# Performance work log

Measured on AMD Instinct MI355X. Metric: run time of the kernel, lower is better.

Reference implementation:

```python
import jax, jax.numpy as jnp
import numpy as np

B, N, D, H = 1, 4096, 1024, 16
HD = D // H  # head_dim = 64


def setup_inputs() -> dict:
    key = jax.random.key(0)
    ks = jax.random.split(key, 5)
    s = 0.02
    return {
        "x": jax.random.normal(ks[0], (B, N, D), dtype=jnp.float32),
        "Wq": jax.random.normal(ks[1], (D, D), dtype=jnp.float32) * s,
        "Wk": jax.random.normal(ks[2], (D, D), dtype=jnp.float32) * s,
        "Wv": jax.random.normal(ks[3], (D, D), dtype=jnp.float32) * s,
        "Wo": jax.random.normal(ks[4], (D, D), dtype=jnp.float32) * s,
        "bo": jnp.zeros((D,), dtype=jnp.float32),
    }


def reference(x, Wq, Wk, Wv, Wo, bo):
    b, n, d = x.shape
    # QKV projections -> [b, h, n, hd]
    def proj(W):
        return jnp.einsum("bnd,de->bne", x, W).reshape(b, n, H, HD).transpose(0, 2, 1, 3)
    q, k, v = proj(Wq), proj(Wk), proj(Wv)
    # Scores [b, h, n, n] with causal mask (matches masked_fill with triu(diag=1))
    scores = jnp.einsum("bhqd,bhkd->bhqk", q, k)
    causal = jnp.tril(jnp.ones((n, n), dtype=bool))
    scores = jnp.where(causal, scores, -jnp.inf)
    attn = jax.nn.softmax(scores / jnp.sqrt(jnp.float32(HD)), axis=-1)
    # dropout p=0.0 -> identity
    ctx = jnp.einsum("bhqk,bhkd->bhqd", attn, v)
    ctx = ctx.transpose(0, 2, 1, 3).reshape(b, n, d)
    return jnp.einsum("bnd,de->bne", ctx, Wo) + bo
```

## Files before the change

kernel.cpp:

```cpp
#include <hip/hip_runtime.h>


#define N_TOK 4096
#define DMODEL 1024
#define NH 16
#define HDIM 64

typedef __bf16 bf16x8 __attribute__((ext_vector_type(8)));
typedef __bf16 bf16x2v __attribute__((ext_vector_type(2)));
typedef short short4v __attribute__((ext_vector_type(4)));
typedef unsigned int uint2v __attribute__((ext_vector_type(2)));
typedef float f32x4 __attribute__((ext_vector_type(4)));

__device__ __forceinline__ unsigned short f2bf(float f) {
  unsigned u = __builtin_bit_cast(unsigned, f);
  u += 0x7FFFu + ((u >> 16) & 1u);
  return (unsigned short)(u >> 16);
}

__device__ __forceinline__ float bf2f(unsigned short u) {
  unsigned x = (unsigned)u << 16;
  return __builtin_bit_cast(float, x);
}

__device__ __forceinline__ unsigned pack2bf(float f0, float f1) {
  unsigned a = __builtin_bit_cast(unsigned, f0);
  unsigned b = __builtin_bit_cast(unsigned, f1);
  a += 0x7FFFu + ((a >> 16) & 1u);
  b += 0x7FFFu + ((b >> 16) & 1u);
  return (a >> 16) | (b & 0xFFFF0000u);
}

__device__ __forceinline__ unsigned packpk(float f0, float f1) {
#if defined(__HIP_DEVICE_COMPILE__) && __has_builtin(__builtin_amdgcn_cvt_pk_bf16_f32)
  bf16x2v r = __builtin_amdgcn_cvt_pk_bf16_f32(f0, f1);
  return __builtin_bit_cast(unsigned, r);
#else
  return pack2bf(f0, f1);
#endif
}

__device__ __forceinline__ float fast_exp2(float x) {
#if defined(__HIP_DEVICE_COMPILE__)
#if __has_builtin(__builtin_amdgcn_exp2f)
  return __builtin_amdgcn_exp2f(x);
#else
  float r;
  asm("v_exp_f32 %0, %1" : "=v"(r) : "v"(x));
  return r;
#endif
#else
  return exp2f(x);
#endif
}

__device__ __forceinline__ f32x4 mfma16x16x16(short4v a, short4v b, f32x4 c) {
#if defined(__HIP_DEVICE_COMPILE__)
#if __has_builtin(__builtin_amdgcn_mfma_f32_16x16x16bf16_1k)
  return __builtin_amdgcn_mfma_f32_16x16x16bf16_1k(a, b, c, 0, 0, 0);
#else
  asm volatile("v_mfma_f32_16x16x16_bf16 %0, %1, %2, %0\n\ts_nop 7\n\ts_nop 1"
               : "+v"(c) : "v"(a), "v"(b));
  return c;
#endif
#else
  return c;
#endif
}

__device__ __forceinline__ void gll16(const unsigned short* g, unsigned short* l) {
#if defined(__HIP_DEVICE_COMPILE__)
  __builtin_amdgcn_global_load_lds((const __attribute__((address_space(1))) void*)g,
                                   (__attribute__((address_space(3))) void*)l, 16, 0, 0);
#endif
}

__global__ __launch_bounds__(256) void prep_kernel(
    const float* __restrict__ x, unsigned short* __restrict__ xb,
    const float* __restrict__ Wq, const float* __restrict__ Wk,
    const float* __restrict__ Wv, const float* __restrict__ Wo,
    unsigned short* __restrict__ Wqt, unsigned short* __restrict__ Wkt,
    unsigned short* __restrict__ Wvt, unsigned short* __restrict__ Wot) {
  const int bx = blockIdx.x;
  if (bx < 4096) {
    const int i = (bx * 256 + threadIdx.x) * 4;
    float4 v = *(const float4*)(x + i);
    ushort4 o;
    o.x = f2bf(v.x); o.y = f2bf(v.y); o.z = f2bf(v.z); o.w = f2bf(v.w);
    *(ushort4*)(xb + i) = o;
    return;
  }
  __shared__ float t[32][33];
  const int r = bx - 4096;
  const int z = r >> 10, rem = r & 1023;
  const int by = rem >> 5, bxx = rem & 31;
  const float* src;
  unsigned short* dst;
  switch (z) {
    case 0: src = Wq; dst = Wqt; break;
    case 1: src = Wk; dst = Wkt; break;
    case 2: src = Wv; dst = Wvt; break;
    default: src = Wo; dst = Wot; break;
  }
  const int tx = threadIdx.x & 31, ty = threadIdx.x >> 5;
  const int xx = bxx * 32 + tx;
  const int y0 = by * 32;
#pragma unroll
  for (int i = 0; i < 32; i += 8) t[ty + i][tx] = src[(y0 + ty + i) * DMODEL + xx];
  __syncthreads();
  const int ox = by * 32 + tx;
  const int oy0 = bxx * 32;
#pragma unroll
  for (int i = 0; i < 32; i += 8) dst[(oy0 + ty + i) * DMODEL + ox] = f2bf(t[tx][ty + i]);
}

__global__ __launch_bounds__(256) void gemm_qkv_kernel(
    const unsigned short* __restrict__ xb,
    const unsigned short* __restrict__ Wqt, const unsigned short* __restrict__ Wkt,
    const unsigned short* __restrict__ Wvt,
    unsigned short* __restrict__ Qg, unsigned short* __restrict__ Kg,
    unsigned short* __restrict__ Vtg) {
  __shared__ __align__(16) char smem[32768];
  const int z = blockIdx.z;
  const unsigned short* Bmat = (z == 0) ? Wqt : ((z == 1) ? Wkt : Wvt);
  const int tid = threadIdx.x, lane = tid & 63, wv = tid >> 6;
  const int quad = lane >> 4, l15 = lane & 15;
  const int wm = wv >> 1, wn = wv & 1;
  const int tm0 = blockIdx.y * 128, tn0 = blockIdx.x * 128;
  const int lrow = lane >> 2, lcol = (lane & 3) * 8;
  const f32x4 zero4 = {0.f, 0.f, 0.f, 0.f};
  f32x4 acc[4][4];
#pragma unroll
  for (int i = 0; i < 4; ++i)
#pragma unroll
    for (int j = 0; j < 4; ++j) acc[i][j] = zero4;

  auto stage = [&](int kb, int b) {
    unsigned short* As = (unsigned short*)(smem + b * 16384);
    unsigned short* Bs = (unsigned short*)(smem + b * 16384 + 8192);
#pragma unroll
    for (int r = 0; r < 2; ++r) {
      const int row0 = r * 64 + wv * 16;
      gll16(&xb[(tm0 + row0 + lrow) * DMODEL + kb + lcol], &As[row0 * 32]);
      gll16(&Bmat[(tn0 + row0 + lrow) * DMODEL + kb + lcol], &Bs[row0 * 32]);
    }
  };

  stage(0, 0);
  stage(32, 1);
  int cur = 0;
#pragma unroll 1
  for (int kb = 0; kb < DMODEL; kb += 32) {
    if (kb + 32 < DMODEL) asm volatile("s_waitcnt vmcnt(4)" ::: "memory");
    else                  asm volatile("s_waitcnt vmcnt(0)" ::: "memory");
    __builtin_amdgcn_s_barrier();
    const unsigned short* As = (const unsigned short*)(smem + cur * 16384);
    const unsigned short* Bs = (const unsigned short*)(smem + cur * 16384 + 8192);
    bf16x8 af[4], bfr[4];
#pragma unroll
    for (int i = 0; i < 4; ++i) {
      af[i]  = *(const bf16x8*)&As[(wm * 64 + i * 16 + l15) * 32 + quad * 8];
      bfr[i] = *(const bf16x8*)&Bs[(wn * 64 + i * 16 + l15) * 32 + quad * 8];
    }
#pragma unroll
    for (int mt = 0; mt < 4; ++mt)
#pragma unroll
      for (int nt = 0; nt < 4; ++nt)
        acc[mt][nt] = __builtin_amdgcn_mfma_f32_16x16x32_bf16(af[mt], bfr[nt], acc[mt][nt], 0, 0, 0);
    if (kb + 64 < DMODEL) {
      __builtin_amdgcn_s_barrier();
      stage(kb + 64, cur);
    }
    cur ^= 1;
  }
  __syncthreads();

  const float qs = 0.125f * 1.44269504088896f;
  if (z < 2) {
#pragma unroll
    for (int mt = 0; mt < 4; ++mt)
#pragma unroll
      for (int nt = 0; nt < 4; ++nt)
#pragma unroll
        for (int r = 0; r < 4; ++r) {
          const int row = tm0 + wm * 64 + mt * 16 + quad * 4 + r;
          const int col = tn0 + wn * 64 + nt * 16 + l15;
          const float v = acc[mt][nt][r];
          const int hh = col >> 6, hd = col & 63;
          if (z == 0) Qg[(hh * N_TOK + row) * HDIM + hd] = f2bf(v * qs);
          else        Kg[(hh * N_TOK + row) * HDIM + hd] = f2bf(v);
        }
  } else {
    unsigned short* Tt = (unsigned short*)smem;
#pragma unroll 1
    for (int p = 0; p < 2; ++p) {
      if (wn == p) {
#pragma unroll
        for (int mt = 0; mt < 4; ++mt)
#pragma unroll
          for (int nt = 0; nt < 4; ++nt) {
            const int c = nt * 16 + l15;
#pragma unroll
            for (int r = 0; r < 4; ++r)
              Tt[c * 132 + wm * 64 + mt * 16 + quad * 4 + r] = f2bf(acc[mt][nt][r]);
          }
      }
      __syncthreads();
      const int c = tid >> 2, seg = tid & 3;
      const int hh = (tn0 + p * 64) >> 6;
      unsigned short* dst = Vtg + hh * (HDIM * N_TOK) + c * N_TOK + tm0 + seg * 32;
      const unsigned short* srcp = &Tt[c * 132 + seg * 32];
#pragma unroll
      for (int j = 0; j < 4; ++j)
        *(uint4*)(dst + j * 8) = *(const uint4*)(srcp + j * 8);
      __syncthreads();
    }
  }
}

#define TRW 68

__device__ static const unsigned char T_TAB[80] = {
    7, 14, 15, 15, 21, 22, 22, 23, 23, 23, 28, 29, 29, 30, 30, 30, 31, 31, 31, 31,
    6, 12, 13, 13, 14, 18, 19, 19, 20, 20, 20, 21, 21, 22, 24, 25, 25, 26, 26, 26,
    27, 27, 27, 27, 28, 28, 28, 29, 29, 30,
    5, 10, 11, 11, 12, 16, 16, 17, 17, 17, 18, 18, 19, 24, 24, 24, 25, 25, 26,
    4, 8, 9, 9, 10, 16,
    3, 8,
    2,
    1,
    0};
__device__ static const unsigned char G_TAB[80] = {
    0, 0, 0, 1, 0, 0, 1, 0, 1, 2, 0, 0, 1, 0, 1, 2, 0, 1, 2, 3,
    0, 0, 0, 1, 1, 0, 0, 1, 0, 1, 2, 1, 2, 2, 0, 0, 1, 0, 1, 2,
    0, 1, 2, 3, 1, 2, 3, 2, 3, 3,
    0, 0, 0, 1, 1, 0, 1, 0, 1, 2, 1, 2, 2, 1, 2, 3, 2, 3, 3,
    0, 0, 0, 1, 1, 2,
    0, 1,
    0,
    0,
    0};
__device__ static const unsigned char PS_TAB[32] = {
    0, 0, 0, 0, 0, 0, 0, 0,
    0, 2, 4, 6, 8, 10, 12, 14,
    16, 19, 22, 25, 28, 31, 34, 37,
    40, 44, 48, 52, 56, 60, 64, 68};

__device__ __forceinline__ unsigned short* part_slot_ptr(
    unsigned short* poA, unsigned short* poB, int slot) {
  return (slot < 384) ? poA + (size_t)slot * 8192
                      : poB + (size_t)(slot - 384) * 8192;
}

__device__ __forceinline__ void stage_kv(
    const unsigned short* __restrict__ Kh, const unsigned short* __restrict__ Vh,
    int kv0, char* buf, int wv, int lane) {
  unsigned short* Ksb = (unsigned short*)buf;
  unsigned short* Vsb = (unsigned short*)(buf + 8192);
  const int r8 = lane >> 3, g = lane & 7;
  const int sw = ((g ^ r8) * 8);
#pragma unroll
  for (int i = 0; i < 2; ++i) {
    const int row = wv * 16 + i * 8;
    gll16(&Kh[(kv0 + row + r8) * HDIM + sw], &Ksb[row * 64]);
    gll16(&Vh[(row + r8) * N_TOK + kv0 + sw], &Vsb[row * 64]);
  }
}

template <bool MASKED>
__device__ __forceinline__ void attn_step(
    int kvs, int qw, int quad, int l15,
    const unsigned short* __restrict__ Ks, const unsigned short* __restrict__ Vs,
    const bf16x8 (&qf)[2][2], f32x4 (&o)[2][4], float (&l_)[2]) {
  const f32x4 zero4 = {0.f, 0.f, 0.f, 0.f};
  const int s = l15 & 7;
  f32x4 c[2][4];
#pragma unroll
  for (int mt = 0; mt < 4; ++mt) {
    const unsigned short* kp = &Ks[(mt * 16 + l15) * 64];
    const int g0 = (quad ^ s) * 8;
    const bf16x8 kf0 = *(const bf16x8*)(kp + g0);
    const bf16x8 kf1 = *(const bf16x8*)(kp + (g0 ^ 32));
#pragma unroll
    for (int qt = 0; qt < 2; ++qt) {
      c[qt][mt] = __builtin_amdgcn_mfma_f32_16x16x32_bf16(kf0, qf[qt][0], zero4, 0, 0, 0);
      c[qt][mt] = __builtin_amdgcn_mfma_f32_16x16x32_bf16(kf1, qf[qt][1], c[qt][mt], 0, 0, 0);
    }
  }
  short4v pb[2][4];
#pragma unroll
  for (int qt = 0; qt < 2; ++qt) {
    const int q = qw + qt * 16 + l15;
    float ls = 0.f;
#pragma unroll
    for (int mt = 0; mt < 4; ++mt) {
      float p[4];
#pragma unroll
      for (int r = 0; r < 4; ++r) {
        float v = c[qt][mt][r];
        if (MASKED) v = ((kvs + mt * 16 + quad * 4 + r) <= q) ? v : -3e38f;
        p[r] = fast_exp2(v);
      }
      ls += (p[0] + p[1]) + (p[2] + p[3]);
      uint2v w;
      w.x = packpk(p[0], p[1]);
      w.y = packpk(p[2], p[3]);
      pb[qt][mt] = __builtin_bit_cast(short4v, w);
    }
    l_[qt] += ls;
  }
#pragma unroll
  for (int mt = 0; mt < 4; ++mt)
#pragma unroll
    for (int dt = 0; dt < 4; ++dt) {
      const int gv = (((2 * mt + (quad >> 1)) ^ s) * 8) + (quad & 1) * 4;
      const short4v vfx = *(const short4v*)&Vs[(dt * 16 + l15) * 64 + gv];
      o[0][dt] = mfma16x16x16(vfx, pb[0][mt], o[0][dt]);
      o[1][dt] = mfma16x16x16(vfx, pb[1][mt], o[1][dt]);
    }
}

__global__ __launch_bounds__(256, 4) void attn_kernel(
    const unsigned short* __restrict__ Qg, const unsigned short* __restrict__ Kg,
    const unsigned short* __restrict__ Vtg, unsigned short* __restrict__ ctx,
    unsigned short* __restrict__ part_oA, unsigned short* __restrict__ part_oB,
    float* __restrict__ part_l) {
  __shared__ __align__(16) char smem[34816];
  const int tid = threadIdx.x, lane = tid & 63, wv = tid >> 6;
  const int quad = lane >> 4, l15 = lane & 15;

  const int xcd = blockIdx.x & 7;
  const int iblk = blockIdx.x >> 3;
  const int h = (xcd << 1) | (iblk & 1);
  const int u = iblk >> 1;
  const int t = T_TAB[u], g = G_TAB[u];
  const int ng = (t >> 3) + 1;
  const int tp1 = t + 1;
  const int gbase = tp1 / ng;
  const int grem = tp1 - gbase * ng;
  const int s0 = g * gbase + (g < grem ? g : grem);
  const int cnt = gbase + (g < grem ? 1 : 0);
  const int mlen = 2 * cnt;
  const bool multi = (t >= 8);
  const int qb = t * 128, qw = qb + wv * 32;

  const unsigned short* Qh = Qg + h * N_TOK * HDIM;
  const unsigned short* Kh = Kg + h * N_TOK * HDIM;
  const unsigned short* Vh = Vtg + h * HDIM * N_TOK;

  bf16x8 qf[2][2];
#pragma unroll
  for (int qt = 0; qt < 2; ++qt)
#pragma unroll
    for (int hh = 0; hh < 2; ++hh)
      qf[qt][hh] = *(const bf16x8*)&Qh[(qw + qt * 16 + l15) * HDIM + hh * 32 + quad * 8];

  const f32x4 zero4 = {0.f, 0.f, 0.f, 0.f};
  f32x4 o[2][4];
#pragma unroll
  for (int qt = 0; qt < 2; ++qt)
#pragma unroll
    for (int dt = 0; dt < 4; ++dt) o[qt][dt] = zero4;
  float l_[2] = {0.f, 0.f};

  const int kvbase = s0 << 7;
  stage_kv(Kh, Vh, kvbase, smem, wv, lane);
  stage_kv(Kh, Vh, kvbase + 64, smem + 16384, wv, lane);
  int cur = 0;
#pragma unroll 1
  for (int mc = 0; mc < mlen; ++mc) {
    const int kv0 = kvbase + mc * 64;
    if (mc + 1 < mlen) asm volatile("s_waitcnt vmcnt(4)" ::: "memory");
    else               asm volatile("s_waitcnt vmcnt(0)" ::: "memory");
    __builtin_amdgcn_s_barrier();
    const unsigned short* Ksb = (const unsigned short*)(smem + cur * 16384);
    const unsigned short* Vsb = (const unsigned short*)(smem + cur * 16384 + 8192);
    if (kv0 <= qw + 31) {
      __builtin_amdgcn_s_setprio(1);
      if (kv0 + 63 <= qw)
        attn_step<false>(kv0, qw, quad, l15, Ksb, Vsb, qf, o, l_);
      else
        attn_step<true>(kv0, qw, quad, l15, Ksb, Vsb, qf, o, l_);
      __builtin_amdgcn_s_setprio(0);
    }
    if (mc + 2 < mlen) {
      __builtin_amdgcn_s_barrier();
      stage_kv(Kh, Vh, kv0 + 128, smem + cur * 16384, wv, lane);
    }
    cur ^= 1;
  }
  __syncthreads();

  float* Tr = (float*)(smem + wv * (16 * TRW * 4));
  const int tq = lane >> 2, seg = lane & 3;
  if (!multi) {
#pragma unroll
    for (int qt = 0; qt < 2; ++qt) {
      float l = l_[qt];
      l += __shfl_xor(l, 16, 64);
      l += __shfl_xor(l, 32, 64);
      const float inv = 1.0f / l;
#pragma unroll
      for (int dt = 0; dt < 4; ++dt) {
        f32x4 v = o[qt][dt] * inv;
        *(f32x4*)&Tr[l15 * TRW + dt * 16 + quad * 4] = v;
      }
      unsigned short* dst = &ctx[(qb + wv * 32 + qt * 16 + tq) * DMODEL + h * HDIM + seg * 16];
      const float* src = &Tr[tq * TRW + seg * 16];
#pragma unroll
      for (int j = 0; j < 2; ++j) {
        const float* s8 = src + j * 8;
        uint4 w;
        w.x = pack2bf(s8[0], s8[1]);
        w.y = pack2bf(s8[2], s8[3]);
        w.z = pack2bf(s8[4], s8[5]);
        w.w = pack2bf(s8[6], s8[7]);
        *(uint4*)(dst + j * 8) = w;
      }
    }
  } else {
    const int slot = h * 72 + PS_TAB[t] + g;
    unsigned short* pobase = part_slot_ptr(part_oA, part_oB, slot);
#pragma unroll
    for (int qt = 0; qt < 2; ++qt) {
      float l = l_[qt];
      l += __shfl_xor(l, 16, 64);
      l += __shfl_xor(l, 32, 64);
      if (quad == 0) part_l[slot * 128 + wv * 32 + qt * 16 + l15] = l;
#pragma unroll
      for (int dt = 0; dt < 4; ++dt)
        *(f32x4*)&Tr[l15 * TRW + dt * 16 + quad * 4] = o[qt][dt];
      unsigned short* dst = pobase + (wv * 32 + qt * 16 + tq) * 64 + seg * 16;
      const float* src = &Tr[tq * TRW + seg * 16];
#pragma unroll
      for (int j = 0; j < 2; ++j) {
        const float* s8 = src + j * 8;
        uint4 w;
        w.x = pack2bf(s8[0], s8[1]);
        w.y = pack2bf(s8[2], s8[3]);
        w.z = pack2bf(s8[4], s8[5]);
        w.w = pack2bf(s8[6], s8[7]);
        *(uint4*)(dst + j * 8) = w;
      }
    }
  }
}

__global__ __launch_bounds__(256) void merge_kernel(
    unsigned short* __restrict__ part_oA, unsigned short* __restrict__ part_oB,
    const float* __restrict__ part_l, unsigned short* __restrict__ ctx) {
  const int b = blockIdx.x;
  const int h = b / 24, tt = b - h * 24;
  const int t = tt + 8;
  const int ng = (t >> 3) + 1;
  const int tid = threadIdx.x;
  const int q = tid >> 1, half = tid & 1;
  const int slot0 = h * 72 + PS_TAB[t];
  float l = 0.f;
  for (int g = 0; g < ng; ++g) l += part_l[(slot0 + g) * 128 + q];
  const float inv = 1.0f / l;
  unsigned short* dst = &ctx[(t * 128 + q) * DMODEL + h * HDIM + half * 32];
#pragma unroll
  for (int j = 0; j < 4; ++j) {
    float acc[8] = {0.f, 0.f, 0.f, 0.f, 0.f, 0.f, 0.f, 0.f};
    for (int g = 0; g < ng; ++g) {
      const unsigned short* po = part_slot_ptr(part_oA, part_oB, slot0 + g);
      const uint4 w = *(const uint4*)(po + q * 64 + half * 32 + j * 8);
      const unsigned short* us = (const unsigned short*)&w;
#pragma unroll
      for (int e = 0; e < 8; ++e) acc[e] += bf2f(us[e]);
    }
    uint4 w;
    w.x = pack2bf(acc[0] * inv, acc[1] * inv);
    w.y = pack2bf(acc[2] * inv, acc[3] * inv);
    w.z = pack2bf(acc[4] * inv, acc[5] * inv);
    w.w = pack2bf(acc[6] * inv, acc[7] * inv);
    *(uint4*)(dst + j * 8) = w;
  }
}

__global__ __launch_bounds__(256) void gemm_out_kernel(
    const unsigned short* __restrict__ ctxb, const unsigned short* __restrict__ Wot,
    const float* __restrict__ bo, float* __restrict__ out) {
  __shared__ __align__(16) char smem[24576];
  const int tid = threadIdx.x, lane = tid & 63, wv = tid >> 6;
  const int quad = lane >> 4, l15 = lane & 15;
  const int wm = wv >> 1, wn = wv & 1;
  const int tm0 = blockIdx.y * 128, tn0 = blockIdx.x * 64;
  const int lrow = lane >> 2, lcol = (lane & 3) * 8;
  const f32x4 zero4 = {0.f, 0.f, 0.f, 0.f};
  f32x4 acc[4][2];
#pragma unroll
  for (int i = 0; i < 4; ++i)
#pragma unroll
    for (int j = 0; j < 2; ++j) acc[i][j] = zero4;

  auto stage = [&](int kb, int b) {
    unsigned short* As = (unsigned short*)(smem + b * 8192);
    unsigned short* Bs = (unsigned short*)(smem + 16384 + b * 4096);
    const int ra = wv * 32;
    gll16(&ctxb[(tm0 + ra + lrow) * DMODEL + kb + lcol], &As[ra * 32]);
    gll16(&ctxb[(tm0 + ra + 16 + lrow) * DMODEL + kb + lcol], &As[(ra + 16) * 32]);
    const int rb = wv * 16;
    gll16(&Wot[(tn0 + rb + lrow) * DMODEL + kb + lcol], &Bs[rb * 32]);
  };
  stage(0, 0);
  stage(32, 1);
  int cur = 0;
#pragma unroll 1
  for (int kb = 0; kb < DMODEL; kb += 32) {
    if (kb + 32 < DMODEL) asm volatile("s_waitcnt vmcnt(3)" ::: "memory");
    else                  asm volatile("s_waitcnt vmcnt(0)" ::: "memory");
    __builtin_amdgcn_s_barrier();
    const unsigned short* As = (const unsigned short*)(smem + cur * 8192);
    const unsigned short* Bs = (const unsigned short*)(smem + 16384 + cur * 4096);
    bf16x8 af[4], bfr[2];
#pragma unroll
    for (int i = 0; i < 4; ++i)
      af[i] = *(const bf16x8*)&As[(wm * 64 + i * 16 + l15) * 32 + quad * 8];
#pragma unroll
    for (int j = 0; j < 2; ++j)
      bfr[j] = *(const bf16x8*)&Bs[(wn * 32 + j * 16 + l15) * 32 + quad * 8];
#pragma unroll
    for (int mt = 0; mt < 4; ++mt)
#pragma unroll
      for (int nt = 0; nt < 2; ++nt)
        acc[mt][nt] = __builtin_amdgcn_mfma_f32_16x16x32_bf16(af[mt], bfr[nt], acc[mt][nt], 0, 0, 0);
    if (kb + 64 < DMODEL) {
      __builtin_amdgcn_s_barrier();
      stage(kb + 64, cur);
    }
    cur ^= 1;
  }
#pragma unroll
  for (int mt = 0; mt < 4; ++mt)
#pragma unroll
    for (int nt = 0; nt < 2; ++nt)
#pragma unroll
      for (int r = 0; r < 4; ++r) {
        const int row = tm0 + wm * 64 + mt * 16 + quad * 4 + r;
        const int col = tn0 + wn * 32 + nt * 16 + l15;
        out[row * DMODEL + col] = acc[mt][nt][r] + bo[col];
      }
}

extern "C" void kernel_launch(void* const* d_in, const int* in_sizes, int n_in,
                              void* d_out, int out_size, void* d_ws, size_t ws_size,
                              hipStream_t stream) {
  const float* x  = (const float*)d_in[0];
  const float* Wq = (const float*)d_in[1];
  const float* Wk = (const float*)d_in[2];
  const float* Wv = (const float*)d_in[3];
  const float* Wo = (const float*)d_in[4];
  const float* bo = (const float*)d_in[5];
  float* out = (float*)d_out;

  char* ws = (char*)d_ws;
  unsigned short* xb  = (unsigned short*)(ws);
  unsigned short* Wqt = (unsigned short*)(ws + 8388608);
  unsigned short* Wkt = (unsigned short*)(ws + 8388608 + 2097152);
  unsigned short* Wvt = (unsigned short*)(ws + 8388608 + 2 * 2097152);
  unsigned short* Wot = (unsigned short*)(ws + 8388608 + 3 * 2097152);
  unsigned short* Qg  = (unsigned short*)(ws + 16777216);
  unsigned short* Kg  = (unsigned short*)(ws + 25165824);
  unsigned short* Vtg = (unsigned short*)(ws + 33554432);
  unsigned short* ctx = xb;
  unsigned short* part_oA = (unsigned short*)(ws + 8388608);
  unsigned short* part_oB = (unsigned short*)(ws + 41943040);
  float* part_l = (float*)(ws + 54525952);

  prep_kernel<<<8192, 256, 0, stream>>>(x, xb, Wq, Wk, Wv, Wo, Wqt, Wkt, Wvt, Wot);
  gemm_qkv_kernel<<<dim3(DMODEL / 128, N_TOK / 128, 3), 256, 0, stream>>>(xb, Wqt, Wkt, Wvt, Qg, Kg, Vtg);
  attn_kernel<<<1280, 256, 0, stream>>>(Qg, Kg, Vtg, ctx, part_oA, part_oB, part_l);
  merge_kernel<<<384, 256, 0, stream>>>(part_oA, part_oB, part_l, ctx);
  gemm_out_kernel<<<dim3(DMODEL / 64, N_TOK / 128), 256, 0, stream>>>(ctx, Wot, bo, out);
}
```

Measured before the change: 206.2 us.

## Fuse x fp32-to-bf16 conversion into QKV GEMM A-tile loading

The separate pass that converts x to bf16 in the prep kernel is removed. The QKV GEMM now loads fp32 x tiles into registers, packs them to bf16 and writes them to LDS, software-pipelined one stage ahead. The weight B tiles keep using global_load_lds. This drops one full read/write round trip of x through HBM and halves the prep launch, but every GEMM block now reads fp32 A data (twice the bytes, repeated across column blocks and z) and spends VALU and LDS writes on the conversion. It also adds a launch_bounds occupancy hint of 3.

Measured after the change: 204.1 us. About the same (-1.0%).

```diff
diff --git a/kernel.cpp b/kernel.cpp
--- a/kernel.cpp
+++ b/kernel.cpp
@@ -76,22 +76,12 @@
 }
 
 __global__ __launch_bounds__(256) void prep_kernel(
-    const float* __restrict__ x, unsigned short* __restrict__ xb,
     const float* __restrict__ Wq, const float* __restrict__ Wk,
     const float* __restrict__ Wv, const float* __restrict__ Wo,
     unsigned short* __restrict__ Wqt, unsigned short* __restrict__ Wkt,
     unsigned short* __restrict__ Wvt, unsigned short* __restrict__ Wot) {
-  const int bx = blockIdx.x;
-  if (bx < 4096) {
-    const int i = (bx * 256 + threadIdx.x) * 4;
-    float4 v = *(const float4*)(x + i);
-    ushort4 o;
-    o.x = f2bf(v.x); o.y = f2bf(v.y); o.z = f2bf(v.z); o.w = f2bf(v.w);
-    *(ushort4*)(xb + i) = o;
-    return;
-  }
   __shared__ float t[32][33];
-  const int r = bx - 4096;
+  const int r = blockIdx.x;
   const int z = r >> 10, rem = r & 1023;
   const int by = rem >> 5, bxx = rem & 31;
   const float* src;
@@ -114,8 +104,8 @@
   for (int i = 0; i < 32; i += 8) dst[(oy0 + ty + i) * DMODEL + ox] = f2bf(t[tx][ty + i]);
 }
 
-__global__ __launch_bounds__(256) void gemm_qkv_kernel(
-    const unsigned short* __restrict__ xb,
+__global__ __launch_bounds__(256, 3) void gemm_qkv_kernel(
+    const float* __restrict__ x,
     const unsigned short* __restrict__ Wqt, const unsigned short* __restrict__ Wkt,
     const unsigned short* __restrict__ Wvt,
     unsigned short* __restrict__ Qg, unsigned short* __restrict__ Kg,
@@ -135,24 +125,45 @@
 #pragma unroll
     for (int j = 0; j < 4; ++j) acc[i][j] = zero4;
 
-  auto stage = [&](int kb, int b) {
+  const int arow = tid >> 1;
+  const int ahalf = (tid & 1) << 4;
+  const float* xrow = x + (size_t)(tm0 + arow) * DMODEL + ahalf;
+  float4 a0, a1, a2, a3;
+  auto issueA = [&](int kb) {
+    const float* p = xrow + kb;
+    a0 = *(const float4*)(p);
+    a1 = *(const float4*)(p + 4);
+    a2 = *(const float4*)(p + 8);
+    a3 = *(const float4*)(p + 12);
+  };
+  auto writeA = [&](int b) {
     unsigned short* As = (unsigned short*)(smem + b * 16384);
+    uint4 w0, w1;
+    w0.x = packpk(a0.x, a0.y); w0.y = packpk(a0.z, a0.w);
+    w0.z = packpk(a1.x, a1.y); w0.w = packpk(a1.z, a1.w);
+    w1.x = packpk(a2.x, a2.y); w1.y = packpk(a2.z, a2.w);
+    w1.z = packpk(a3.x, a3.y); w1.w = packpk(a3.z, a3.w);
+    *(uint4*)&As[arow * 32 + ahalf] = w0;
+    *(uint4*)&As[arow * 32 + ahalf + 8] = w1;
+  };
+  auto stageB = [&](int kb, int b) {
     unsigned short* Bs = (unsigned short*)(smem + b * 16384 + 8192);
 #pragma unroll
     for (int r = 0; r < 2; ++r) {
       const int row0 = r * 64 + wv * 16;
-      gll16(&xb[(tm0 + row0 + lrow) * DMODEL + kb + lcol], &As[row0 * 32]);
       gll16(&Bmat[(tn0 + row0 + lrow) * DMODEL + kb + lcol], &Bs[row0 * 32]);
     }
   };
 
-  stage(0, 0);
-  stage(32, 1);
+  stageB(0, 0);
+  stageB(32, 1);
+  issueA(0);
+  writeA(0);
+  issueA(32);
   int cur = 0;
 #pragma unroll 1
   for (int kb = 0; kb < DMODEL; kb += 32) {
-    if (kb + 32 < DMODEL) asm volatile("s_waitcnt vmcnt(4)" ::: "memory");
-    else                  asm volatile("s_waitcnt vmcnt(0)" ::: "memory");
+    asm volatile("s_waitcnt lgkmcnt(0)" ::: "memory");
     __builtin_amdgcn_s_barrier();
     const unsigned short* As = (const unsigned short*)(smem + cur * 16384);
     const unsigned short* Bs = (const unsigned short*)(smem + cur * 16384 + 8192);
@@ -167,10 +178,9 @@
 #pragma unroll
       for (int nt = 0; nt < 4; ++nt)
         acc[mt][nt] = __builtin_amdgcn_mfma_f32_16x16x32_bf16(af[mt], bfr[nt], acc[mt][nt], 0, 0, 0);
-    if (kb + 64 < DMODEL) {
-      __builtin_amdgcn_s_barrier();
-      stage(kb + 64, cur);
-    }
+    __builtin_amdgcn_s_barrier();
+    if (kb + 32 < DMODEL) writeA(cur ^ 1);
+    if (kb + 64 < DMODEL) { stageB(kb + 64, cur); issueA(kb + 64); }
     cur ^= 1;
   }
   __syncthreads();
@@ -556,7 +566,6 @@
   float* out = (float*)d_out;
 
   char* ws = (char*)d_ws;
-  unsigned short* xb  = (unsigned short*)(ws);
   unsigned short* Wqt = (unsigned short*)(ws + 8388608);
   unsigned short* Wkt = (unsigned short*)(ws + 8388608 + 2097152);
   unsigned short* Wvt = (unsigned short*)(ws + 8388608 + 2 * 2097152);
@@ -564,13 +573,13 @@
   unsigned short* Qg  = (unsigned short*)(ws + 16777216);
   unsigned short* Kg  = (unsigned short*)(ws + 25165824);
   unsigned short* Vtg = (unsigned short*)(ws + 33554432);
-  unsigned short* ctx = xb;
+  unsigned short* ctx = (unsigned short*)(ws);
   unsigned short* part_oA = (unsigned short*)(ws + 8388608);
   unsigned short* part_oB = (unsigned short*)(ws + 41943040);
   float* part_l = (float*)(ws + 54525952);
 
-  prep_kernel<<<8192, 256, 0, stream>>>(x, xb, Wq, Wk, Wv, Wo, Wqt, Wkt, Wvt, Wot);
-  gemm_qkv_kernel<<<dim3(DMODEL / 128, N_TOK / 128, 3), 256, 0, stream>>>(xb, Wqt, Wkt, Wvt, Qg, Kg, Vtg);
+  prep_kernel<<<4096, 256, 0, stream>>>(Wq, Wk, Wv, Wo, Wqt, Wkt, Wvt, Wot);
+  gemm_qkv_kernel<<<dim3(DMODEL / 128, N_TOK / 128, 3), 256, 0, stream>>>(x, Wqt, Wkt, Wvt, Qg, Kg, Vtg);
   attn_kernel<<<1280, 256, 0, stream>>>(Qg, Kg, Vtg, ctx, part_oA, part_oB, part_l);
   merge_kernel<<<384, 256, 0, stream>>>(part_oA, part_oB, part_l, ctx);
   gemm_out_kernel<<<dim3(DMODEL / 64, N_TOK / 128), 256, 0, stream>>>(ctx, Wot, bo, out);
```
